# Kernel optimization log

Measured on AMD Instinct MI355X. Metric: run time of the kernel, lower is better.

Reference implementation:

```python
import jax, jax.numpy as jnp
import numpy as np

HEADS = 16
DIM_HEAD = 64


def setup_inputs() -> dict:
    key = jax.random.key(0)
    k1, k2, k3 = jax.random.split(key, 3)
    b, n, dim = 4, 2048, 1024
    inner = HEADS * DIM_HEAD  # 1024
    x = jax.random.normal(k1, (b, n, dim), dtype=jnp.float32)
    # Dense weights, scaled like Glorot-ish init to keep softmax well-behaved
    w_qkv = jax.random.normal(k2, (dim, 3 * inner), dtype=jnp.float32) * (dim ** -0.5)
    w_out = jax.random.normal(k3, (inner, dim), dtype=jnp.float32) * (inner ** -0.5)
    b_out = jnp.zeros((dim,), dtype=jnp.float32)
    return {"x": x, "w_qkv": w_qkv, "w_out": w_out, "b_out": b_out}


def reference(x, w_qkv, w_out, b_out):
    b, n, dim = x.shape
    scale = DIM_HEAD ** -0.5
    qkv = x @ w_qkv  # [b, n, 3*h*d]
    q, k, v = jnp.split(qkv, 3, axis=-1)
    # 'b n (h d) -> b h n d'
    split_heads = lambda t: t.reshape(b, n, HEADS, DIM_HEAD).transpose(0, 2, 1, 3)
    q, k, v = split_heads(q), split_heads(k), split_heads(v)
    sim = jnp.einsum('bhid,bhjd->bhij', q, k) * scale  # [b, h, n, n]
    attn = jax.nn.softmax(sim, axis=-1)
    out = jnp.einsum('bhij,bhjd->bhid', attn, v)  # [b, h, n, d]
    out = out.transpose(0, 2, 1, 3).reshape(b, n, HEADS * DIM_HEAD)
    return out @ w_out + b_out  # dropout rate 0.0 -> identity
```

## Files before the change

kernel.cpp:

```cpp
#include <hip/hip_runtime.h>
#include <cstdint>

#define HEADS 16
#define DH 64
#define SEQ 2048
#define BATCH 4
#define DIM 1024
#define MTOT (BATCH*SEQ)
#define NQKV (3*DIM)

typedef short bf16x8 __attribute__((ext_vector_type(8)));
typedef float f32x4 __attribute__((ext_vector_type(4)));
typedef float f32x16 __attribute__((ext_vector_type(16)));

__device__ __forceinline__ unsigned short f2bf(float f) {
  union { float fv; unsigned int u; } c; c.fv = f;
  unsigned int u = c.u;
  u += 0x7FFFu + ((u >> 16) & 1u);
  return (unsigned short)(u >> 16);
}

__device__ __forceinline__ unsigned int cvtpk(float lo, float hi) {
  unsigned int r;
  asm("v_cvt_pk_bf16_f32 %0, %1, %2" : "=v"(r) : "v"(lo), "v"(hi));
  return r;
}

__device__ __forceinline__ f32x4 mfma16(bf16x8 a, bf16x8 b, f32x4 c) {
  return __builtin_amdgcn_mfma_f32_16x16x32_bf16(a, b, c, 0, 0, 0);
}
__device__ __forceinline__ f32x16 mfma32(bf16x8 a, bf16x8 b, f32x16 c) {
  return __builtin_amdgcn_mfma_f32_32x32x16_bf16(a, b, c, 0, 0, 0);
}

typedef const __attribute__((address_space(1))) unsigned int* gas_ptr;
typedef __attribute__((address_space(3))) unsigned int* las_ptr;
__device__ __forceinline__ void gl2lds16(const void* g, void* l) {
  __builtin_amdgcn_global_load_lds((gas_ptr)g, (las_ptr)l, 16, 0, 0);
}

#define QSCALE 0.18033688011112042f

__global__ __launch_bounds__(256) void cast_f32_bf16(
    const float* __restrict__ in, unsigned short* __restrict__ out, int n4) {
  int i = blockIdx.x * blockDim.x + threadIdx.x;
  if (i >= n4) return;
  float4 v = reinterpret_cast<const float4*>(in)[i];
  uint2 o;
  o.x = (unsigned int)f2bf(v.x) | ((unsigned int)f2bf(v.y) << 16);
  o.y = (unsigned int)f2bf(v.z) | ((unsigned int)f2bf(v.w) << 16);
  reinterpret_cast<uint2*>(out)[i] = o;
}

__global__ __launch_bounds__(256) void transpose_cast(
    const float* __restrict__ in, unsigned short* __restrict__ out, int R, int C) {
  __shared__ float tile[32][33];
  int c0 = blockIdx.x * 32, r0 = blockIdx.y * 32;
  int tx = threadIdx.x & 31, ty = threadIdx.x >> 5;
  for (int i = 0; i < 32; i += 8)
    tile[ty + i][tx] = in[(size_t)(r0 + ty + i) * C + c0 + tx];
  __syncthreads();
  for (int i = 0; i < 32; i += 8)
    out[(size_t)(c0 + ty + i) * R + r0 + tx] = f2bf(tile[tx][ty + i]);
}

__global__ __launch_bounds__(256) void transpose_v(
    const unsigned short* __restrict__ V, unsigned short* __restrict__ Vt) {
  __shared__ unsigned short tile[64][72];
  int n0 = blockIdx.x * 64;
  size_t base = (size_t)blockIdx.y * SEQ * DH;
  int t = threadIdx.x;
  int r = t >> 2, c = (t & 3) * 8;
  *(uint4*)&tile[r][c]      = *(const uint4*)&V[base + (size_t)(n0 + r) * DH + c];
  *(uint4*)&tile[r][c + 32] = *(const uint4*)&V[base + (size_t)(n0 + r) * DH + c + 32];
  __syncthreads();
#pragma unroll
  for (int p = 0; p < 2; p++) {
    alignas(16) unsigned short tmp[8];
#pragma unroll
    for (int i = 0; i < 8; i++) tmp[i] = tile[c + p * 32 + i][r];
    *(uint4*)&Vt[base + (size_t)r * SEQ + n0 + c + p * 32] = *(uint4*)tmp;
  }
}

#define BM 128
#define BN 128
#define BK 32
#define LDT 32

__global__ __launch_bounds__(256) void gemm_qkv(
    const unsigned short* __restrict__ A, const unsigned short* __restrict__ Bt,
    unsigned short* __restrict__ Q, unsigned short* __restrict__ K,
    unsigned short* __restrict__ V) {
  __shared__ unsigned short sA[BM * LDT];
  __shared__ unsigned short sB[BN * LDT];
  const int KD = 1024;
  int m0 = blockIdx.y * BM;
  int n0 = blockIdx.x * BN;
  int t = threadIdx.x;
  int lane = t & 63, w = t >> 6;
  int wm = (w >> 1) * 64, wn = (w & 1) * 64;
  int fr = lane & 15, fq = (lane >> 4) * 8;

  const unsigned short* gA = &A[(size_t)(m0 + w * 16 + (lane >> 2)) * KD + (lane & 3) * 8];
  const unsigned short* gB = &Bt[(size_t)(n0 + w * 16 + (lane >> 2)) * KD + (lane & 3) * 8];
  char* lA = (char*)sA + w * 1024;
  char* lB = (char*)sB + w * 1024;

  f32x4 acc[4][4];
#pragma unroll
  for (int i = 0; i < 4; i++)
#pragma unroll
    for (int j = 0; j < 4; j++) { f32x4 z = {0.f, 0.f, 0.f, 0.f}; acc[i][j] = z; }

  for (int k0 = 0; k0 < KD; k0 += BK) {
    gl2lds16(gA + k0, lA);
    gl2lds16(gA + (size_t)64 * KD + k0, lA + 4096);
    gl2lds16(gB + k0, lB);
    gl2lds16(gB + (size_t)64 * KD + k0, lB + 4096);
    __syncthreads();
    bf16x8 af[4], bfr[4];
#pragma unroll
    for (int mt = 0; mt < 4; mt++)
      af[mt] = *reinterpret_cast<const bf16x8*>(&sA[(wm + mt * 16 + fr) * LDT + fq]);
#pragma unroll
    for (int nt = 0; nt < 4; nt++)
      bfr[nt] = *reinterpret_cast<const bf16x8*>(&sB[(wn + nt * 16 + fr) * LDT + fq]);
#pragma unroll
    for (int mt = 0; mt < 4; mt++)
#pragma unroll
      for (int nt = 0; nt < 4; nt++)
        acc[mt][nt] = mfma16(af[mt], bfr[nt], acc[mt][nt]);
    __syncthreads();
  }
  int rowq = (lane >> 4) * 4;
#pragma unroll
  for (int mt = 0; mt < 4; mt++)
#pragma unroll
    for (int nt = 0; nt < 4; nt++)
#pragma unroll
      for (int r = 0; r < 4; r++) {
        int m = m0 + wm + mt * 16 + rowq + r;
        int ncol = n0 + wn + nt * 16 + fr;
        int which = ncol >> 10;
        int hd = ncol & 1023;
        int b = m >> 11, nrow = m & 2047;
        float v = acc[mt][nt][r];
        if (which == 0) v *= QSCALE;
        unsigned short* dst = (which == 0) ? Q : (which == 1 ? K : V);
        size_t idx = ((size_t)(b * HEADS + (hd >> 6)) * SEQ + nrow) * DH + (hd & 63);
        dst[idx] = f2bf(v);
      }
}

__global__ __launch_bounds__(256) void gemm_out(
    const unsigned short* __restrict__ A, const unsigned short* __restrict__ Bt,
    const float* __restrict__ bias, float* __restrict__ C) {
  __shared__ unsigned short sA[BM * LDT];
  __shared__ unsigned short sB[BN * LDT];
  const int KD = 1024;
  int m0 = blockIdx.y * BM;
  int n0 = blockIdx.x * BN;
  int t = threadIdx.x;
  int lane = t & 63, w = t >> 6;
  int wm = (w >> 1) * 64, wn = (w & 1) * 64;
  int fr = lane & 15, fq = (lane >> 4) * 8;

  const unsigned short* gA = &A[(size_t)(m0 + w * 16 + (lane >> 2)) * KD + (lane & 3) * 8];
  const unsigned short* gB = &Bt[(size_t)(n0 + w * 16 + (lane >> 2)) * KD + (lane & 3) * 8];
  char* lA = (char*)sA + w * 1024;
  char* lB = (char*)sB + w * 1024;

  f32x4 acc[4][4];
#pragma unroll
  for (int i = 0; i < 4; i++)
#pragma unroll
    for (int j = 0; j < 4; j++) { f32x4 z = {0.f, 0.f, 0.f, 0.f}; acc[i][j] = z; }

  for (int k0 = 0; k0 < KD; k0 += BK) {
    gl2lds16(gA + k0, lA);
    gl2lds16(gA + (size_t)64 * KD + k0, lA + 4096);
    gl2lds16(gB + k0, lB);
    gl2lds16(gB + (size_t)64 * KD + k0, lB + 4096);
    __syncthreads();
    bf16x8 af[4], bfr[4];
#pragma unroll
    for (int mt = 0; mt < 4; mt++)
      af[mt] = *reinterpret_cast<const bf16x8*>(&sA[(wm + mt * 16 + fr) * LDT + fq]);
#pragma unroll
    for (int nt = 0; nt < 4; nt++)
      bfr[nt] = *reinterpret_cast<const bf16x8*>(&sB[(wn + nt * 16 + fr) * LDT + fq]);
#pragma unroll
    for (int mt = 0; mt < 4; mt++)
#pragma unroll
      for (int nt = 0; nt < 4; nt++)
        acc[mt][nt] = mfma16(af[mt], bfr[nt], acc[mt][nt]);
    __syncthreads();
  }
  int rowq = (lane >> 4) * 4;
#pragma unroll
  for (int mt = 0; mt < 4; mt++)
#pragma unroll
    for (int nt = 0; nt < 4; nt++)
#pragma unroll
      for (int r = 0; r < 4; r++) {
        int m = m0 + wm + mt * 16 + rowq + r;
        int ncol = n0 + wn + nt * 16 + fr;
        C[(size_t)m * DIM + ncol] = acc[mt][nt][r] + bias[ncol];
      }
}

#define LDA 68

__global__ __launch_bounds__(256, 4) void attention(
    const unsigned short* __restrict__ Qg, const unsigned short* __restrict__ Kg,
    const unsigned short* __restrict__ Vtg, unsigned short* __restrict__ Og) {
  __shared__ unsigned short smem[2 * 64 * 72];
  unsigned short* sK  = smem;
  unsigned short* sVt = smem + 64 * LDA;

  int gid = blockIdx.x + 16 * (blockIdx.y + 16 * blockIdx.z);
  int qb   = (gid >> 3) & 15;
  int pair = ((gid & 7) << 3) | (gid >> 7);
  int h = pair & 15, b = pair >> 4;

  size_t base = (size_t)(b * HEADS + h) * SEQ * DH;
  const unsigned short* Q = Qg + base;
  const unsigned short* K = Kg + base;
  const unsigned short* Vt = Vtg + base;
  int t = threadIdx.x, lane = t & 63, w = t >> 6;
  int m = lane & 31, kh = lane >> 5;
  int q0 = qb * 128 + w * 32;

  bf16x8 qf[4];
#pragma unroll
  for (int kt = 0; kt < 4; kt++)
    qf[kt] = *reinterpret_cast<const bf16x8*>(
        &Q[(size_t)(q0 + m) * DH + kt * 16 + kh * 8]);

  f32x16 oaccT[2];
#pragma unroll
  for (int dh = 0; dh < 2; dh++)
#pragma unroll
    for (int i = 0; i < 16; i++) oaccT[dh][i] = 0.f;
  float rs = 0.f;

  int sr = t >> 2, sc = (t & 3) * 8;

  for (int j0 = 0; j0 < SEQ; j0 += 64) {
    {
      uint4 a0 = *(const uint4*)&K[(size_t)(j0 + sr) * DH + sc];
      uint4 a1 = *(const uint4*)&K[(size_t)(j0 + sr) * DH + sc + 32];
      uint4 b0 = *(const uint4*)&Vt[(size_t)sr * SEQ + j0 + sc];
      uint4 b1 = *(const uint4*)&Vt[(size_t)sr * SEQ + j0 + sc + 32];
      unsigned short* pk0 = &sK[sr * LDA + sc];
      unsigned short* pk1 = &sK[sr * LDA + sc + 32];
      unsigned short* pv0 = &sVt[sr * LDA + sc];
      unsigned short* pv1 = &sVt[sr * LDA + sc + 32];
      *(uint2*)pk0       = make_uint2(a0.x, a0.y);
      *(uint2*)(pk0 + 4) = make_uint2(a0.z, a0.w);
      *(uint2*)pk1       = make_uint2(a1.x, a1.y);
      *(uint2*)(pk1 + 4) = make_uint2(a1.z, a1.w);
      *(uint2*)pv0       = make_uint2(b0.x, b0.y);
      *(uint2*)(pv0 + 4) = make_uint2(b0.z, b0.w);
      *(uint2*)pv1       = make_uint2(b1.x, b1.y);
      *(uint2*)(pv1 + 4) = make_uint2(b1.z, b1.w);
    }
    __syncthreads();

    unsigned int pp[8][2];
#pragma unroll
    for (int jt = 0; jt < 2; jt++) {
      bf16x8 kf[4];
#pragma unroll
      for (int kt = 0; kt < 4; kt++) {
        union { uint2 u[2]; bf16x8 v; } kc;
        const unsigned short* p = &sK[(jt * 32 + m) * LDA + (2 * kt + kh) * 8];
        kc.u[0] = *(const uint2*)p;
        kc.u[1] = *(const uint2*)(p + 4);
        kf[kt] = kc.v;
      }
      f32x16 s;
#pragma unroll
      for (int i = 0; i < 16; i++) s[i] = 0.f;
#pragma unroll
      for (int kt = 0; kt < 4; kt++)
        s = mfma32(kf[kt], qf[kt], s);
      float e[16];
#pragma unroll
      for (int i = 0; i < 16; i++) e[i] = __builtin_amdgcn_exp2f(s[i]);
      float t0 = (e[0] + e[1]) + (e[2] + e[3]);
      float t1 = (e[4] + e[5]) + (e[6] + e[7]);
      float t2 = (e[8] + e[9]) + (e[10] + e[11]);
      float t3 = (e[12] + e[13]) + (e[14] + e[15]);
      rs += (t0 + t1) + (t2 + t3);
#pragma unroll
      for (int sl = 0; sl < 4; sl++) {
        pp[4 * jt + sl][0] = cvtpk(e[4 * sl + 0], e[4 * sl + 1]);
        pp[4 * jt + sl][1] = cvtpk(e[4 * sl + 2], e[4 * sl + 3]);
      }
    }

#pragma unroll
    for (int kb = 0; kb < 4; kb++) {
#pragma unroll
      for (int dh = 0; dh < 2; dh++) {
        union { uint2 u[2]; bf16x8 v; } ac;
        const unsigned short* p = &sVt[(32 * dh + m) * LDA + 16 * kb + 4 * kh];
        ac.u[0] = *(const uint2*)p;
        ac.u[1] = *(const uint2*)(p + 8);
        union { unsigned int u[4]; bf16x8 v; } bc;
        bc.u[0] = pp[2 * kb][0];
        bc.u[1] = pp[2 * kb][1];
        bc.u[2] = pp[2 * kb + 1][0];
        bc.u[3] = pp[2 * kb + 1][1];
        oaccT[dh] = mfma32(ac.v, bc.v, oaccT[dh]);
      }
    }
    __syncthreads();
  }

  float inv;
  {
    float tot = rs + __shfl_xor(rs, 32);
    inv = 1.0f / tot;
  }

  unsigned int* ew = (unsigned int*)smem + (size_t)w * 32 * 36;
#pragma unroll
  for (int dh = 0; dh < 2; dh++)
#pragma unroll
    for (int sl = 0; sl < 4; sl++) {
      unsigned int u0 = cvtpk(oaccT[dh][4 * sl + 0] * inv, oaccT[dh][4 * sl + 1] * inv);
      unsigned int u1 = cvtpk(oaccT[dh][4 * sl + 2] * inv, oaccT[dh][4 * sl + 3] * inv);
      uint2 pk; pk.x = u0; pk.y = u1;
      *(uint2*)&ew[m * 36 + 16 * dh + 4 * sl + 2 * kh] = pk;
    }
  {
    int mr = lane >> 3, ch = lane & 7;
#pragma unroll
    for (int it = 0; it < 4; it++) {
      uint4 vv = *(const uint4*)&ew[(8 * it + mr) * 36 + ch * 4];
      int n = q0 + 8 * it + mr;
      *(uint4*)&Og[((size_t)(b * SEQ + n)) * DIM + h * DH + ch * 8] = vv;
    }
  }
}

extern "C" void kernel_launch(void* const* d_in, const int* in_sizes, int n_in,
                              void* d_out, int out_size, void* d_ws, size_t ws_size,
                              hipStream_t stream) {
  const float* x     = (const float*)d_in[0];
  const float* w_qkv = (const float*)d_in[1];
  const float* w_out = (const float*)d_in[2];
  const float* b_out = (const float*)d_in[3];
  float* out = (float*)d_out;

  char* ws = (char*)d_ws;
  unsigned short* xb     = (unsigned short*)ws; ws += (size_t)MTOT * DIM * 2;
  unsigned short* wqkv_t = (unsigned short*)ws; ws += (size_t)NQKV * DIM * 2;
  unsigned short* wout_t = (unsigned short*)ws; ws += (size_t)DIM * DIM * 2;
  unsigned short* qb_    = (unsigned short*)ws; ws += (size_t)BATCH * HEADS * SEQ * DH * 2;
  unsigned short* kb_    = (unsigned short*)ws; ws += (size_t)BATCH * HEADS * SEQ * DH * 2;
  unsigned short* vb_    = (unsigned short*)ws; ws += (size_t)BATCH * HEADS * SEQ * DH * 2;
  unsigned short* attnb  = (unsigned short*)ws; ws += (size_t)MTOT * DIM * 2;
  unsigned short* vt_    = xb;

  cast_f32_bf16<<<(MTOT * DIM / 4 + 255) / 256, 256, 0, stream>>>(x, xb, MTOT * DIM / 4);
  transpose_cast<<<dim3(NQKV / 32, DIM / 32), 256, 0, stream>>>(w_qkv, wqkv_t, DIM, NQKV);
  transpose_cast<<<dim3(DIM / 32, DIM / 32), 256, 0, stream>>>(w_out, wout_t, DIM, DIM);

  gemm_qkv<<<dim3(NQKV / BN, MTOT / BM), 256, 0, stream>>>(xb, wqkv_t, qb_, kb_, vb_);

  transpose_v<<<dim3(SEQ / 64, BATCH * HEADS), 256, 0, stream>>>(vb_, vt_);

  attention<<<dim3(SEQ / 128, HEADS, BATCH), 256, 0, stream>>>(qb_, kb_, vt_, attnb);

  gemm_out<<<dim3(DIM / BN, MTOT / BM), 256, 0, stream>>>(attnb, wout_t, b_out, out);
}
```

Baseline: 269.5 us.

## Double GEMM K-tile, XOR-swizzle LDS, reorder blocks, replace bf16 pack asm

Both projection GEMMs now stage a 64-wide K slice per iteration instead of 32. This halves the number of barrier pairs and global-to-LDS rounds. The LDS layout is XOR-swizzled to avoid bank conflicts, and block IDs are remapped so that groups of 8 consecutive blocks share operand rows for better L2 reuse. Separately, the attention kernel's inline-asm v_cvt_pk_bf16_f32 is replaced by an integer add-and-shift bf16 pack, which rounds slightly differently and may take more ALU instructions.

```diff
diff --git a/kernel.cpp b/kernel.cpp
--- a/kernel.cpp
+++ b/kernel.cpp
@@ -20,10 +20,9 @@
   return (unsigned short)(u >> 16);
 }
 
-__device__ __forceinline__ unsigned int cvtpk(float lo, float hi) {
-  unsigned int r;
-  asm("v_cvt_pk_bf16_f32 %0, %1, %2" : "=v"(r) : "v"(lo), "v"(hi));
-  return r;
+__device__ __forceinline__ unsigned int pkbf(float lo, float hi) {
+  union { float fv; unsigned int u; } a, b; a.fv = lo; b.fv = hi;
+  return ((a.u + 0x8000u) >> 16) | ((b.u + 0x8000u) & 0xFFFF0000u);
 }
 
 __device__ __forceinline__ f32x4 mfma16(bf16x8 a, bf16x8 b, f32x4 c) {
@@ -85,25 +84,28 @@
 
 #define BM 128
 #define BN 128
-#define BK 32
-#define LDT 32
+#define BK 64
 
 __global__ __launch_bounds__(256) void gemm_qkv(
     const unsigned short* __restrict__ A, const unsigned short* __restrict__ Bt,
     unsigned short* __restrict__ Q, unsigned short* __restrict__ K,
     unsigned short* __restrict__ V) {
-  __shared__ unsigned short sA[BM * LDT];
-  __shared__ unsigned short sB[BN * LDT];
+  __shared__ unsigned short sA[BM * BK];
+  __shared__ unsigned short sB[BN * BK];
   const int KD = 1024;
-  int m0 = blockIdx.y * BM;
-  int n0 = blockIdx.x * BN;
+  int gid = blockIdx.x + 24 * blockIdx.y;
+  int swz = (gid & 7) * 192 + (gid >> 3);
+  int m0 = (swz / 24) * BM;
+  int n0 = (swz % 24) * BN;
   int t = threadIdx.x;
   int lane = t & 63, w = t >> 6;
   int wm = (w >> 1) * 64, wn = (w & 1) * 64;
-  int fr = lane & 15, fq = (lane >> 4) * 8;
-
-  const unsigned short* gA = &A[(size_t)(m0 + w * 16 + (lane >> 2)) * KD + (lane & 3) * 8];
-  const unsigned short* gB = &Bt[(size_t)(n0 + w * 16 + (lane >> 2)) * KD + (lane & 3) * 8];
+  int fr = lane & 15, fg = lane >> 4;
+
+  int srow = w * 8 + (lane >> 3);
+  int scol = ((lane & 7) ^ (lane >> 3)) * 8;
+  const unsigned short* gA = &A[(size_t)(m0 + srow) * KD + scol];
+  const unsigned short* gB = &Bt[(size_t)(n0 + srow) * KD + scol];
   char* lA = (char*)sA + w * 1024;
   char* lB = (char*)sB + w * 1024;
 
@@ -114,23 +116,29 @@
     for (int j = 0; j < 4; j++) { f32x4 z = {0.f, 0.f, 0.f, 0.f}; acc[i][j] = z; }
 
   for (int k0 = 0; k0 < KD; k0 += BK) {
-    gl2lds16(gA + k0, lA);
-    gl2lds16(gA + (size_t)64 * KD + k0, lA + 4096);
-    gl2lds16(gB + k0, lB);
-    gl2lds16(gB + (size_t)64 * KD + k0, lB + 4096);
-    __syncthreads();
-    bf16x8 af[4], bfr[4];
-#pragma unroll
-    for (int mt = 0; mt < 4; mt++)
-      af[mt] = *reinterpret_cast<const bf16x8*>(&sA[(wm + mt * 16 + fr) * LDT + fq]);
-#pragma unroll
-    for (int nt = 0; nt < 4; nt++)
-      bfr[nt] = *reinterpret_cast<const bf16x8*>(&sB[(wn + nt * 16 + fr) * LDT + fq]);
-#pragma unroll
-    for (int mt = 0; mt < 4; mt++)
+#pragma unroll
+    for (int i = 0; i < 4; i++) {
+      gl2lds16(gA + (size_t)i * 32 * KD + k0, lA + i * 4096);
+      gl2lds16(gB + (size_t)i * 32 * KD + k0, lB + i * 4096);
+    }
+    __syncthreads();
+#pragma unroll
+    for (int ks = 0; ks < 2; ks++) {
+      bf16x8 af[4], bfr[4];
+#pragma unroll
+      for (int mt = 0; mt < 4; mt++)
+        af[mt] = *reinterpret_cast<const bf16x8*>(
+            &sA[(wm + mt * 16 + fr) * BK + (((ks * 4 + fg) ^ (fr & 7)) * 8)]);
 #pragma unroll
       for (int nt = 0; nt < 4; nt++)
-        acc[mt][nt] = mfma16(af[mt], bfr[nt], acc[mt][nt]);
+        bfr[nt] = *reinterpret_cast<const bf16x8*>(
+            &sB[(wn + nt * 16 + fr) * BK + (((ks * 4 + fg) ^ (fr & 7)) * 8)]);
+#pragma unroll
+      for (int mt = 0; mt < 4; mt++)
+#pragma unroll
+        for (int nt = 0; nt < 4; nt++)
+          acc[mt][nt] = mfma16(af[mt], bfr[nt], acc[mt][nt]);
+    }
     __syncthreads();
   }
   int rowq = (lane >> 4) * 4;
@@ -156,18 +164,22 @@
 __global__ __launch_bounds__(256) void gemm_out(
     const unsigned short* __restrict__ A, const unsigned short* __restrict__ Bt,
     const float* __restrict__ bias, float* __restrict__ C) {
-  __shared__ unsigned short sA[BM * LDT];
-  __shared__ unsigned short sB[BN * LDT];
+  __shared__ unsigned short sA[BM * BK];
+  __shared__ unsigned short sB[BN * BK];
   const int KD = 1024;
-  int m0 = blockIdx.y * BM;
-  int n0 = blockIdx.x * BN;
+  int gid = blockIdx.x + 8 * blockIdx.y;
+  int swz = (gid & 7) * 64 + (gid >> 3);
+  int m0 = (swz / 8) * BM;
+  int n0 = (swz % 8) * BN;
   int t = threadIdx.x;
   int lane = t & 63, w = t >> 6;
   int wm = (w >> 1) * 64, wn = (w & 1) * 64;
-  int fr = lane & 15, fq = (lane >> 4) * 8;
-
-  const unsigned short* gA = &A[(size_t)(m0 + w * 16 + (lane >> 2)) * KD + (lane & 3) * 8];
-  const unsigned short* gB = &Bt[(size_t)(n0 + w * 16 + (lane >> 2)) * KD + (lane & 3) * 8];
+  int fr = lane & 15, fg = lane >> 4;
+
+  int srow = w * 8 + (lane >> 3);
+  int scol = ((lane & 7) ^ (lane >> 3)) * 8;
+  const unsigned short* gA = &A[(size_t)(m0 + srow) * KD + scol];
+  const unsigned short* gB = &Bt[(size_t)(n0 + srow) * KD + scol];
   char* lA = (char*)sA + w * 1024;
   char* lB = (char*)sB + w * 1024;
 
@@ -178,23 +190,29 @@
     for (int j = 0; j < 4; j++) { f32x4 z = {0.f, 0.f, 0.f, 0.f}; acc[i][j] = z; }
 
   for (int k0 = 0; k0 < KD; k0 += BK) {
-    gl2lds16(gA + k0, lA);
-    gl2lds16(gA + (size_t)64 * KD + k0, lA + 4096);
-    gl2lds16(gB + k0, lB);
-    gl2lds16(gB + (size_t)64 * KD + k0, lB + 4096);
-    __syncthreads();
-    bf16x8 af[4], bfr[4];
-#pragma unroll
-    for (int mt = 0; mt < 4; mt++)
-      af[mt] = *reinterpret_cast<const bf16x8*>(&sA[(wm + mt * 16 + fr) * LDT + fq]);
-#pragma unroll
-    for (int nt = 0; nt < 4; nt++)
-      bfr[nt] = *reinterpret_cast<const bf16x8*>(&sB[(wn + nt * 16 + fr) * LDT + fq]);
-#pragma unroll
-    for (int mt = 0; mt < 4; mt++)
+#pragma unroll
+    for (int i = 0; i < 4; i++) {
+      gl2lds16(gA + (size_t)i * 32 * KD + k0, lA + i * 4096);
+      gl2lds16(gB + (size_t)i * 32 * KD + k0, lB + i * 4096);
+    }
+    __syncthreads();
+#pragma unroll
+    for (int ks = 0; ks < 2; ks++) {
+      bf16x8 af[4], bfr[4];
+#pragma unroll
+      for (int mt = 0; mt < 4; mt++)
+        af[mt] = *reinterpret_cast<const bf16x8*>(
+            &sA[(wm + mt * 16 + fr) * BK + (((ks * 4 + fg) ^ (fr & 7)) * 8)]);
 #pragma unroll
       for (int nt = 0; nt < 4; nt++)
-        acc[mt][nt] = mfma16(af[mt], bfr[nt], acc[mt][nt]);
+        bfr[nt] = *reinterpret_cast<const bf16x8*>(
+            &sB[(wn + nt * 16 + fr) * BK + (((ks * 4 + fg) ^ (fr & 7)) * 8)]);
+#pragma unroll
+      for (int mt = 0; mt < 4; mt++)
+#pragma unroll
+        for (int nt = 0; nt < 4; nt++)
+          acc[mt][nt] = mfma16(af[mt], bfr[nt], acc[mt][nt]);
+    }
     __syncthreads();
   }
   int rowq = (lane >> 4) * 4;
@@ -296,8 +314,8 @@
       rs += (t0 + t1) + (t2 + t3);
 #pragma unroll
       for (int sl = 0; sl < 4; sl++) {
-        pp[4 * jt + sl][0] = cvtpk(e[4 * sl + 0], e[4 * sl + 1]);
-        pp[4 * jt + sl][1] = cvtpk(e[4 * sl + 2], e[4 * sl + 3]);
+        pp[4 * jt + sl][0] = pkbf(e[4 * sl + 0], e[4 * sl + 1]);
+        pp[4 * jt + sl][1] = pkbf(e[4 * sl + 2], e[4 * sl + 3]);
       }
     }
 
@@ -331,8 +349,8 @@
   for (int dh = 0; dh < 2; dh++)
 #pragma unroll
     for (int sl = 0; sl < 4; sl++) {
-      unsigned int u0 = cvtpk(oaccT[dh][4 * sl + 0] * inv, oaccT[dh][4 * sl + 1] * inv);
-      unsigned int u1 = cvtpk(oaccT[dh][4 * sl + 2] * inv, oaccT[dh][4 * sl + 3] * inv);
+      unsigned int u0 = pkbf(oaccT[dh][4 * sl + 0] * inv, oaccT[dh][4 * sl + 1] * inv);
+      unsigned int u1 = pkbf(oaccT[dh][4 * sl + 2] * inv, oaccT[dh][4 * sl + 3] * inv);
       uint2 pk; pk.x = u0; pk.y = u1;
       *(uint2*)&ew[m * 36 + 16 * dh + 4 * sl + 2 * kh] = pk;
     }
```

New measurement: 279.4 us. 3.7% more time.
